# Kernel optimization log

Hardware: AMD Instinct MI355X
Metric: run time of the kernel (lower is better)

The kernel has to match this reference:

```python
import jax, jax.numpy as jnp
import numpy as np

N = 50000          # nodes
E = 800000         # edges
H = 64             # hidden_dim == node_embedding_dim (heads=1)
ED = 32            # edge_embedding_dim
L = 3              # num_layers - 1 TransformerConv layers
G = 256            # graphs in batch
NODE_CAT = 42
EDGE_CAT = 10
OUT = 32
SCALE = 1.0 / np.sqrt(H)


def segment_softmax(logits, seg, num_segments):
    mx = jax.ops.segment_max(logits, seg, num_segments=num_segments)
    e = jnp.exp(logits - mx[seg])
    denom = jax.ops.segment_sum(e, seg, num_segments=num_segments)
    return e / denom[seg]


def setup_inputs() -> dict:
    key = jax.random.key(0)
    ks = jax.random.split(key, 16)

    def init(k, shape, fan_in):
        return (jax.random.normal(k, shape, jnp.float32) / np.sqrt(fan_in))

    inp = {}
    inp["x"] = jax.random.randint(ks[0], (N,), 0, NODE_CAT)
    inp["edge_index"] = jax.random.randint(ks[1], (2, E), 0, N)
    inp["edge_attr"] = jax.random.randint(ks[2], (E,), 0, EDGE_CAT)
    inp["batch"] = jnp.sort(jax.random.randint(ks[3], (N,), 0, G))

    inp["node_emb"] = init(ks[4], (NODE_CAT, H), 1)
    inp["edge_emb"] = init(ks[5], (EDGE_CAT, ED), 1)
    # stacked per-layer TransformerConv params (input dim is H for all layers
    # since node_embedding_dim == hidden_dim)
    inp["Wq"] = init(ks[6], (L, H, H), H)
    inp["Wk"] = init(ks[7], (L, H, H), H)
    inp["Wv"] = init(ks[8], (L, H, H), H)
    inp["We"] = init(ks[9], (L, ED, H), ED)   # lin_edge, bias=False in PyG
    inp["Wskip"] = init(ks[10], (L, H, H), H)
    inp["bq"] = jnp.zeros((L, H), jnp.float32)
    inp["bk"] = jnp.zeros((L, H), jnp.float32)
    inp["bv"] = jnp.zeros((L, H), jnp.float32)
    inp["bskip"] = jnp.zeros((L, H), jnp.float32)
    # attentional aggregation readout
    inp["gate_W"] = init(ks[11], (H, 1), H)
    inp["gate_b"] = jnp.zeros((1,), jnp.float32)
    inp["out_W"] = init(ks[12], (H, OUT), H)
    inp["out_b"] = jnp.zeros((OUT,), jnp.float32)
    return inp


def reference(x, edge_index, edge_attr, batch, node_emb, edge_emb,
              Wq, Wk, Wv, We, Wskip, bq, bk, bv, bskip,
              gate_W, gate_b, out_W, out_b):
    src, dst = edge_index[0], edge_index[1]
    h = node_emb[x]            # [N, H] node embedding lookup
    e_feat = edge_emb[edge_attr]  # [E, ED] edge embedding lookup

    for l in range(L):
        q = h @ Wq[l] + bq[l]          # [N, H]
        k = h @ Wk[l] + bk[l]
        v = h @ Wv[l] + bv[l]
        e = e_feat @ We[l]             # [E, H]
        k_j = k[src] + e               # key_j += lin_edge(edge_attr)
        alpha = jnp.sum(q[dst] * k_j, axis=-1) * SCALE   # [E]
        a = segment_softmax(alpha, dst, N)               # softmax over dst nbhd
        msg = (v[src] + e) * a[:, None]                  # [E, H]
        agg = jax.ops.segment_sum(msg, dst, num_segments=N)
        h = jax.nn.relu(agg + h @ Wskip[l] + bskip[l])   # root/skip + ReLU

    # AttentionalAggregation: gate = gate_nn(x); x = nn(x); softmax gate per graph
    gate = (h @ gate_W + gate_b)[:, 0]   # [N]
    y = h @ out_W + out_b                # [N, OUT]
    g = segment_softmax(gate, batch, G)  # [N]
    return jax.ops.segment_sum(g[:, None] * y, batch, num_segments=G)  # [G, OUT]
```

## Files before the change

kernel.cpp:

```cpp
#include <hip/hip_runtime.h>
#include <hip/hip_bf16.h>

#define N_NODES 50000
#define N_EDGES 800000
#define H 64
#define ED 32
#define LAYERS 3
#define NGRAPH 256
#define OUTD 32
#define SCALE 0.125f
#define NCAT 42

#define BNODES 128
#define NBUCK 391
#define NB_HISTB 256
#define EPB (N_EDGES / NB_HISTB)

#define FB_HIST 256
#define FB_TE   8
#define FB_GB   2
#define FB_WB   192
#define FB_TAB  NCAT
#define NB_FRONT (FB_HIST + FB_TE + FB_GB + FB_WB + FB_TAB)

#define NB_SCAN   98
#define NB_AGG    3125
#define PKCAP     768

typedef __attribute__((ext_vector_type(8))) short bf16x8;
typedef __attribute__((ext_vector_type(4))) float f32x4;
typedef unsigned short ushort_t;

__device__ __forceinline__ unsigned f2bf(float f) {
    unsigned u = __float_as_uint(f);
    return (u + 0x7FFFu + ((u >> 16) & 1u)) >> 16;
}

__device__ __forceinline__ float radd16(float x) {
    x += __int_as_float(__builtin_amdgcn_update_dpp(0, __float_as_int(x), 0xB1, 0xF, 0xF, true));
    x += __int_as_float(__builtin_amdgcn_update_dpp(0, __float_as_int(x), 0x4E, 0xF, 0xF, true));
    x += __int_as_float(__builtin_amdgcn_update_dpp(0, __float_as_int(x), 0x124, 0xF, 0xF, true));
    x += __int_as_float(__builtin_amdgcn_update_dpp(0, __float_as_int(x), 0x128, 0xF, 0xF, true));
    return x;
}

__device__ __forceinline__ void build_bstart(const int* __restrict__ tot,
                                             int* bst, int* part, int t) {
    int u0 = t * 2, u1 = t * 2 + 1;
    int a0 = (u0 < NBUCK) ? tot[u0] : 0;
    int a1 = (u1 < NBUCK) ? tot[u1] : 0;
    part[t] = a0 + a1;
    __syncthreads();
    for (int off = 1; off < 256; off <<= 1) {
        int add = (t >= off) ? part[t - off] : 0;
        __syncthreads();
        part[t] += add;
        __syncthreads();
    }
    int excl = part[t] - (a0 + a1);
    if (u0 < NBUCK) bst[u0] = excl;
    if (u1 < NBUCK) bst[u1] = excl + a0;
    if (t == 0) bst[NBUCK] = N_EDGES;
    __syncthreads();
}

__global__ __launch_bounds__(256) void k_front(
    const int* __restrict__ x, const float* __restrict__ node_emb,
    const float* __restrict__ edge_emb, const float* __restrict__ We, float* __restrict__ te,
    const int* __restrict__ ei, int* __restrict__ hist,
    const int* __restrict__ batch, int* __restrict__ gs,
    const float* __restrict__ Wq, const float* __restrict__ Wk,
    const float* __restrict__ Wv, const float* __restrict__ Wsk,
    const float* __restrict__ bq, const float* __restrict__ bk,
    const float* __restrict__ bv, const float* __restrict__ bsk,
    ushort_t* __restrict__ wb16,
    unsigned* __restrict__ tqs, unsigned* __restrict__ tkv)
{
    __shared__ int lh[NBUCK];
    __shared__ float tb[4][64];
    int b = blockIdx.x, t = threadIdx.x;
    if (b < FB_HIST) {
        for (int i = t; i < NBUCK; i += 256) lh[i] = 0;
        __syncthreads();
        const int* dstp = ei + N_EDGES + b * EPB;
        for (int i = t; i < EPB; i += 256)
            atomicAdd(&lh[dstp[i] >> 7], 1);
        __syncthreads();
        for (int i = t; i < NBUCK; i += 256) hist[i * NB_HISTB + b] = lh[i];
    } else if (b < FB_HIST + FB_TE) {
        int i = (b - FB_HIST) * 256 + t;
        if (i < LAYERS * 10 * H) {
            int c = i & 63;
            int cat = (i >> 6) % 10;
            int l = i / (10 * H);
            float acc = 0.f;
            for (int d = 0; d < ED; d++)
                acc += edge_emb[cat * ED + d] * We[((size_t)l * ED + d) * H + c];
            te[i] = acc;
        }
    } else if (b < FB_HIST + FB_TE + FB_GB) {
        int g = (b - FB_HIST - FB_TE) * 256 + t;
        if (g <= NGRAPH) {
            int lo = 0, hi = N_NODES;
            while (lo < hi) {
                int mid = (lo + hi) >> 1;
                if (batch[mid] < g) lo = mid + 1; else hi = mid;
            }
            gs[g] = lo;
        }
    } else if (b < FB_HIST + FB_TE + FB_GB + FB_WB) {
        int g = (b - FB_HIST - FB_TE - FB_GB) * 256 + t;
        int l = g >> 14;
        int rem = g & 16383;
        int c_id = rem >> 11;
        int rr = (rem >> 3) & 255;
        int j = rem & 7;
        int mat = rr >> 6, n = rr & 63;
        int k = ((c_id >> 2) << 5) + ((c_id & 3) << 3) + j;
        const float* Wm = (mat == 0) ? Wq : (mat == 1) ? Wk : (mat == 2) ? Wv : Wsk;
        wb16[g] = (ushort_t)f2bf(Wm[(size_t)l * 4096 + k * 64 + n]);
    } else {
        int cat = b - (FB_HIST + FB_TE + FB_GB + FB_WB);
        int mat = t >> 6, c = t & 63;
        const float* Wm = (mat == 0) ? Wq : (mat == 1) ? Wk : (mat == 2) ? Wv : Wsk;
        const float* bm = (mat == 0) ? bq : (mat == 1) ? bk : (mat == 2) ? bv : bsk;
        float acc = bm[c];
        for (int k = 0; k < H; k++)
            acc += node_emb[cat * H + k] * Wm[k * 64 + c];
        tb[mat][c] = acc;
        __syncthreads();
        if (t < 64) {
            tqs[cat * 64 + t] = f2bf(tb[0][t]) | (f2bf(tb[3][t]) << 16);
            tkv[cat * 64 + t] = f2bf(tb[2][t]) | (f2bf(tb[1][t]) << 16);
        }
    }
}

__global__ __launch_bounds__(256) void k_scan(int* __restrict__ hist, int* __restrict__ tot)
{
    __shared__ int sv[256];
    int sb = blockIdx.x, t = threadIdx.x;
    for (int r = 0; r < 4; r++) {
        int u = sb * 4 + r;
        if (u < NBUCK) {
            int v = hist[u * NB_HISTB + t];
            sv[t] = v;
            __syncthreads();
            for (int off = 1; off < 256; off <<= 1) {
                int add = (t >= off) ? sv[t - off] : 0;
                __syncthreads();
                sv[t] += add;
                __syncthreads();
            }
            int incl = sv[t];
            hist[u * NB_HISTB + t] = incl - v;
            if (t == 255) tot[u] = incl;
            __syncthreads();
        }
    }
}

__global__ __launch_bounds__(256) void k_scatter(
    const int* __restrict__ ei, const int* __restrict__ ea, const int* __restrict__ x,
    const int* __restrict__ hist, const int* __restrict__ tot,
    int* __restrict__ pmid)
{
    __shared__ int bst[NBUCK + 1];
    __shared__ int part[256];
    __shared__ int curS[NBUCK];
    int b = blockIdx.x, t = threadIdx.x;
    build_bstart(tot, bst, part, t);
    for (int u = t; u < NBUCK; u += 256)
        curS[u] = bst[u] + hist[u * NB_HISTB + b];
    __syncthreads();
    int e0 = b * EPB;
    for (int i = t; i < EPB; i += 256) {
        int e = e0 + i;
        int src = ei[e], dst = ei[N_EDGES + e], cat = ea[e];
        int xs = x[src];
        int pos = atomicAdd(&curS[dst >> 7], 1);
        pmid[pos] = src | ((cat * NCAT + xs) << 16) | ((dst & 127) << 25);
    }
}

__global__ __launch_bounds__(256) void k_final(
    const int* __restrict__ pmid, const int* __restrict__ tot,
    int* __restrict__ packed, int* __restrict__ row_start, int* __restrict__ row_end)
{
    __shared__ int bst[NBUCK + 1];
    __shared__ int part[256];
    __shared__ int cnt[BNODES];
    __shared__ int scan_s[BNODES];
    int b = blockIdx.x, t = threadIdx.x;
    build_bstart(tot, bst, part, t);
    int beg = bst[b], end = bst[b + 1];
    if (t < BNODES) cnt[t] = 0;
    __syncthreads();
    for (int e = beg + t; e < end; e += 256)
        atomicAdd(&cnt[((unsigned)pmid[e] >> 25) & 127], 1);
    __syncthreads();
    if (t < BNODES) scan_s[t] = cnt[t];
    __syncthreads();
    for (int off = 1; off < BNODES; off <<= 1) {
        int add = (t >= off && t < BNODES) ? scan_s[t - off] : 0;
        __syncthreads();
        if (t < BNODES) scan_s[t] += add;
        __syncthreads();
    }
    if (t < BNODES) {
        int c = cnt[t];
        int excl = scan_s[t] - c;
        int node = b * BNODES + t;
        if (node < N_NODES) {
            row_start[node] = beg + excl;
            row_end[node] = beg + excl + c;
        }
        cnt[t] = beg + excl;
    }
    __syncthreads();
    for (int e = beg + t; e < end; e += 256) {
        int p = pmid[e];
        int pos = atomicAdd(&cnt[((unsigned)p >> 25) & 127], 1);
        packed[pos] = p & 0x1FFFFFF;
    }
}

struct EdgeLd { uint4 kv; float4 t; };
__device__ __forceinline__ float edge_dot(const EdgeLd& e, const float4& q4) {
    float p;
    p = (__uint_as_float(e.kv.x & 0xFFFF0000u) + e.t.x) * q4.x;
    p = fmaf(__uint_as_float(e.kv.y & 0xFFFF0000u) + e.t.y, q4.y, p);
    p = fmaf(__uint_as_float(e.kv.z & 0xFFFF0000u) + e.t.z, q4.z, p);
    p = fmaf(__uint_as_float(e.kv.w & 0xFFFF0000u) + e.t.w, q4.w, p);
    return radd16(p) * SCALE;
}
__device__ __forceinline__ float4 edge_val(const EdgeLd& e) {
    float4 v;
    v.x = __uint_as_float(e.kv.x << 16) + e.t.x;
    v.y = __uint_as_float(e.kv.y << 16) + e.t.y;
    v.z = __uint_as_float(e.kv.z << 16) + e.t.z;
    v.w = __uint_as_float(e.kv.w << 16) + e.t.w;
    return v;
}

template<int MODE>
__device__ __forceinline__ void agg_body(
    const int* __restrict__ row_start, const int* __restrict__ row_end,
    const int* __restrict__ packed, const int* __restrict__ x,
    const unsigned* __restrict__ qs_in, const unsigned* __restrict__ kv_in,
    const unsigned* __restrict__ tqs, const unsigned* __restrict__ tkv,
    const float* __restrict__ te,
    const ushort_t* __restrict__ wbn, const float* __restrict__ bqn,
    const float* __restrict__ bkn, const float* __restrict__ bvn,
    const float* __restrict__ bsn,
    unsigned* __restrict__ qs_out, unsigned* __restrict__ kv_out,
    float* __restrict__ hf, const float* __restrict__ gW,
    const float* __restrict__ gb, float* __restrict__ gate,
    float* tel, ushort_t* hs16, int* pkl)
{
    int t = threadIdx.x, bid = blockIdx.x;
    int wave = t >> 6, lane = t & 63;
    int g = lane >> 4, i16 = lane & 15;
    int dst = bid * 16 + wave * 4 + g;
    int beg = row_start[dst], end = row_end[dst];
    int beg0 = row_start[bid * 16];
    int cnt = row_end[bid * 16 + 15] - beg0;
    bool use_lds = (cnt <= PKCAP);
    for (int i = t; i < 640; i += 256) tel[i] = te[i];
    if (use_lds) for (int i = t; i < cnt; i += 256) pkl[i] = packed[beg0 + i];
    uint4 uq;
    if constexpr (MODE == 0)
        uq = *(const uint4*)(tqs + (x[dst] << 6) + (i16 << 2));
    else
        uq = *(const uint4*)(qs_in + (size_t)dst * 64 + (i16 << 2));
    __syncthreads();
    float4 q4, s4;
    q4.x = __uint_as_float(uq.x << 16); s4.x = __uint_as_float(uq.x & 0xFFFF0000u);
    q4.y = __uint_as_float(uq.y << 16); s4.y = __uint_as_float(uq.y & 0xFFFF0000u);
    q4.z = __uint_as_float(uq.z << 16); s4.z = __uint_as_float(uq.z & 0xFFFF0000u);
    q4.w = __uint_as_float(uq.w << 16); s4.w = __uint_as_float(uq.w & 0xFFFF0000u);
    float m = -1e30f, l = 0.f;
    float4 acc = {0.f, 0.f, 0.f, 0.f};

    auto eload = [&](int pkt) {
        EdgeLd r;
        unsigned catx = ((unsigned)pkt >> 16) & 0x1FFu;
        int cat = (int)((catx * 1561u) >> 16);
        r.t = *(const float4*)(tel + (cat << 6) + (i16 << 2));
        if constexpr (MODE == 0) {
            int xc = (int)catx - cat * NCAT;
            r.kv = *(const uint4*)(tkv + (xc << 6) + (i16 << 2));
        } else {
            int src = pkt & 0xFFFF;
            r.kv = *(const uint4*)(kv_in + ((size_t)src << 6) + (i16 << 2));
        }
        return r;
    };
    auto run = [&](auto PKT) {
        int e = beg;
        for (; e + 3 < end; e += 4) {
            int p0 = PKT(e), p1 = PKT(e + 1), p2 = PKT(e + 2), p3 = PKT(e + 3);
            EdgeLd e0 = eload(p0), e1 = eload(p1), e2 = eload(p2), e3 = eload(p3);
            float a0 = edge_dot(e0, q4), a1 = edge_dot(e1, q4);
            float a2 = edge_dot(e2, q4), a3 = edge_dot(e3, q4);
            float mn = fmaxf(m, fmaxf(fmaxf(a0, a1), fmaxf(a2, a3)));
            float corr = __expf(m - mn);
            float w0 = __expf(a0 - mn), w1 = __expf(a1 - mn);
            float w2 = __expf(a2 - mn), w3 = __expf(a3 - mn);
            float4 v0 = edge_val(e0), v1 = edge_val(e1), v2 = edge_val(e2), v3 = edge_val(e3);
            acc.x = fmaf(w0, v0.x, fmaf(w1, v1.x, fmaf(w2, v2.x, fmaf(w3, v3.x, acc.x * corr))));
            acc.y = fmaf(w0, v0.y, fmaf(w1, v1.y, fmaf(w2, v2.y, fmaf(w3, v3.y, acc.y * corr))));
            acc.z = fmaf(w0, v0.z, fmaf(w1, v1.z, fmaf(w2, v2.z, fmaf(w3, v3.z, acc.z * corr))));
            acc.w = fmaf(w0, v0.w, fmaf(w1, v1.w, fmaf(w2, v2.w, fmaf(w3, v3.w, acc.w * corr))));
            l = fmaf(l, corr, (w0 + w1) + (w2 + w3));
            m = mn;
        }
        for (; e < end; e++) {
            EdgeLd e0 = eload(PKT(e));
            float a = edge_dot(e0, q4);
            float mn = fmaxf(m, a);
            float corr = __expf(m - mn);
            float w = __expf(a - mn);
            float4 v4 = edge_val(e0);
            acc.x = fmaf(w, v4.x, acc.x * corr);
            acc.y = fmaf(w, v4.y, acc.y * corr);
            acc.z = fmaf(w, v4.z, acc.z * corr);
            acc.w = fmaf(w, v4.w, acc.w * corr);
            l = fmaf(l, corr, w);
            m = mn;
        }
    };
    if (use_lds) run([&](int e) { return pkl[e - beg0]; });
    else         run([&](int e) { return packed[e]; });

    float inv = (l > 0.f) ? 1.f / l : 0.f;
    float4 hv;
    hv.x = fmaxf(acc.x * inv + s4.x, 0.f);
    hv.y = fmaxf(acc.y * inv + s4.y, 0.f);
    hv.z = fmaxf(acc.z * inv + s4.z, 0.f);
    hv.w = fmaxf(acc.w * inv + s4.w, 0.f);
    if constexpr (MODE == 2) {
        *(float4*)(hf + (size_t)dst * H + (i16 << 2)) = hv;
        float4 g4 = *(const float4*)(gW + (i16 << 2));
        float p = hv.x * g4.x + hv.y * g4.y + hv.z * g4.z + hv.w * g4.w;
        p = radd16(p);
        if (i16 == 0) gate[dst] = p + gb[0];
    } else {
        uint2 hp;
        hp.x = f2bf(hv.x) | (f2bf(hv.y) << 16);
        hp.y = f2bf(hv.z) | (f2bf(hv.w) << 16);
        *(uint2*)(hs16 + (((wave * 4 + g) << 6) + (i16 << 2))) = hp;
        __syncthreads();
        int n16 = lane & 15, quad = lane >> 4;
        f32x4 oacc[4];
        #pragma unroll
        for (int i = 0; i < 4; i++) oacc[i] = (f32x4){0.f, 0.f, 0.f, 0.f};
        #pragma unroll
        for (int kb = 0; kb < 2; kb++) {
            bf16x8 afr = *(const bf16x8*)(hs16 + ((n16 << 6) + kb * 32 + quad * 8));
            #pragma unroll
            for (int mat = 0; mat < 4; mat++) {
                int ct = mat * 4 + wave;
                const bf16x8* bp = (const bf16x8*)(wbn + (((kb * 4 + quad) << 11) + ((ct * 16 + n16) << 3)));
                oacc[mat] = __builtin_amdgcn_mfma_f32_16x16x32_bf16(afr, *bp, oacc[mat], 0, 0, 0);
            }
        }
        int col = (wave << 4) + n16;
        float bQ = bqn[col], bK = bkn[col], bV = bvn[col], bS = bsn[col];
        int nb = bid * 16 + quad * 4;
        #pragma unroll
        for (int r = 0; r < 4; r++) {
            qs_out[(size_t)(nb + r) * 64 + col] = f2bf(oacc[0][r] + bQ) | (f2bf(oacc[3][r] + bS) << 16);
            kv_out[(size_t)(nb + r) * 64 + col] = f2bf(oacc[2][r] + bV) | (f2bf(oacc[1][r] + bK) << 16);
        }
    }
}

__global__ __launch_bounds__(256, 6) void k_agg0(
    const int* __restrict__ row_start, const int* __restrict__ row_end,
    const int* __restrict__ packed, const int* __restrict__ x,
    const unsigned* __restrict__ tqs, const unsigned* __restrict__ tkv,
    const float* __restrict__ te,
    const ushort_t* __restrict__ wbn, const float* __restrict__ bqn,
    const float* __restrict__ bkn, const float* __restrict__ bvn,
    const float* __restrict__ bsn,
    unsigned* __restrict__ qs_out, unsigned* __restrict__ kv_out)
{
    __shared__ float tel[640];
    __shared__ ushort_t hs16[1024];
    __shared__ int pkl[PKCAP];
    agg_body<0>(row_start, row_end, packed, x, nullptr, nullptr, tqs, tkv, te,
                wbn, bqn, bkn, bvn, bsn, qs_out, kv_out,
                nullptr, nullptr, nullptr, nullptr, tel, hs16, pkl);
}

__global__ __launch_bounds__(256, 6) void k_agg1(
    const int* __restrict__ row_start, const int* __restrict__ row_end,
    const int* __restrict__ packed,
    const unsigned* __restrict__ qs_in, const unsigned* __restrict__ kv_in,
    const float* __restrict__ te,
    const ushort_t* __restrict__ wbn, const float* __restrict__ bqn,
    const float* __restrict__ bkn, const float* __restrict__ bvn,
    const float* __restrict__ bsn,
    unsigned* __restrict__ qs_out, unsigned* __restrict__ kv_out)
{
    __shared__ float tel[640];
    __shared__ ushort_t hs16[1024];
    __shared__ int pkl[PKCAP];
    agg_body<1>(row_start, row_end, packed, nullptr, qs_in, kv_in, nullptr, nullptr, te,
                wbn, bqn, bkn, bvn, bsn, qs_out, kv_out,
                nullptr, nullptr, nullptr, nullptr, tel, hs16, pkl);
}

__global__ __launch_bounds__(256, 6) void k_agg2(
    const int* __restrict__ row_start, const int* __restrict__ row_end,
    const int* __restrict__ packed,
    const unsigned* __restrict__ qs_in, const unsigned* __restrict__ kv_in,
    const float* __restrict__ te,
    float* __restrict__ hf, const float* __restrict__ gW,
    const float* __restrict__ gb, float* __restrict__ gate)
{
    __shared__ float tel[640];
    __shared__ int pkl[PKCAP];
    agg_body<2>(row_start, row_end, packed, nullptr, qs_in, kv_in, nullptr, nullptr, te,
                nullptr, nullptr, nullptr, nullptr, nullptr, nullptr, nullptr,
                hf, gW, gb, gate, tel, nullptr, pkl);
}

__global__ __launch_bounds__(256) void k_readout2(
    const float* __restrict__ h, const float* __restrict__ oW,
    const float* __restrict__ ob, const float* __restrict__ gate,
    const int* __restrict__ gs, float* __restrict__ out)
{
    __shared__ float hs[8][H + 1];
    __shared__ float red[256];
    __shared__ float den_s[8];
    __shared__ float gmax_s, den_tot;
    int t = threadIdx.x;
    int g = blockIdx.x;
    int ln = t >> 5, o = t & 31;
    float wreg[H];
    #pragma unroll
    for (int i = 0; i < H; i++) wreg[i] = oW[i * OUTD + o];
    int beg = gs[g], end = gs[g + 1];
    float mx = -INFINITY;
    for (int n = beg + t; n < end; n += 256) mx = fmaxf(mx, gate[n]);
    red[t] = mx;
    __syncthreads();
    for (int sft = 128; sft > 0; sft >>= 1) {
        if (t < sft) red[t] = fmaxf(red[t], red[t + sft]);
        __syncthreads();
    }
    if (t == 0) gmax_s = red[0];
    __syncthreads();
    float gm = gmax_s;
    float acc = 0.f, den = 0.f;
    for (int n0 = beg; n0 < end; n0 += 8) {
        __syncthreads();
        for (int i = t; i < 8 * H; i += 256) {
            int r = i >> 6, c = i & 63;
            int n = n0 + r;
            hs[r][c] = (n < end) ? h[(size_t)n * H + c] : 0.f;
        }
        __syncthreads();
        int n = n0 + ln;
        if (n < end) {
            float wt = __expf(gate[n] - gm);
            float d0 = 0.f;
            #pragma unroll
            for (int i = 0; i < H; i++) d0 += hs[ln][i] * wreg[i];
            acc += wt * d0;
            if (o == 0) den += wt;
        }
    }
    __syncthreads();
    red[t] = acc;
    if (o == 0) den_s[ln] = den;
    __syncthreads();
    for (int sft = 4; sft >= 1; sft >>= 1) {
        if (ln < sft) red[t] += red[t + sft * 32];
        __syncthreads();
    }
    if (t == 0) {
        float dt = 0.f;
        #pragma unroll
        for (int i = 0; i < 8; i++) dt += den_s[i];
        den_tot = dt;
    }
    __syncthreads();
    if (ln == 0) {
        float dt = den_tot;
        out[g * OUTD + o] = (dt > 0.f) ? red[o] / dt + ob[o] : 0.f;
    }
}

extern "C" void kernel_launch(void* const* d_in, const int* in_sizes, int n_in,
                              void* d_out, int out_size, void* d_ws, size_t ws_size,
                              hipStream_t stream)
{
    const int* x        = (const int*)d_in[0];
    const int* ei       = (const int*)d_in[1];
    const int* ea       = (const int*)d_in[2];
    const int* batch    = (const int*)d_in[3];
    const float* node_emb = (const float*)d_in[4];
    const float* edge_emb = (const float*)d_in[5];
    const float* Wq    = (const float*)d_in[6];
    const float* Wk    = (const float*)d_in[7];
    const float* Wv    = (const float*)d_in[8];
    const float* We    = (const float*)d_in[9];
    const float* Wskip = (const float*)d_in[10];
    const float* bq    = (const float*)d_in[11];
    const float* bk    = (const float*)d_in[12];
    const float* bv    = (const float*)d_in[13];
    const float* bskip = (const float*)d_in[14];
    const float* gate_W = (const float*)d_in[15];
    const float* gate_b = (const float*)d_in[16];
    const float* out_W  = (const float*)d_in[17];
    const float* out_b  = (const float*)d_in[18];
    float* out = (float*)d_out;

    const size_t NH = (size_t)N_NODES * H;
    float* ws   = (float*)d_ws;
    unsigned* qs_a = (unsigned*)ws;
    unsigned* kv_a = qs_a + NH;
    unsigned* qs_b = kv_a + NH;
    unsigned* kv_b = qs_b + NH;
    float* hf32 = (float*)(kv_b + NH);
    float* te   = hf32 + NH;
    float* gate = te + LAYERS * 10 * H;
    int* row_start = (int*)(gate + N_NODES);
    int* row_end   = row_start + N_NODES;
    int* packed    = row_end + N_NODES;
    int* pmid      = packed + N_EDGES;
    int* hist      = pmid + N_EDGES;
    int* tot       = hist + NBUCK * NB_HISTB;
    int* gs        = tot + NBUCK;
    unsigned* tqs  = (unsigned*)(gs + NGRAPH + 1);
    unsigned* tkv  = tqs + FB_TAB * 64;
    ushort_t* wb16 = (ushort_t*)(tkv + FB_TAB * 64);

    k_front<<<NB_FRONT, 256, 0, stream>>>(x, node_emb, edge_emb, We, te, ei, hist, batch, gs,
                                          Wq, Wk, Wv, Wskip, bq, bk, bv, bskip, wb16, tqs, tkv);
    k_scan<<<NB_SCAN, 256, 0, stream>>>(hist, tot);
    k_scatter<<<NB_HISTB, 256, 0, stream>>>(ei, ea, x, hist, tot, pmid);
    k_final<<<NBUCK, 256, 0, stream>>>(pmid, tot, packed, row_start, row_end);

    k_agg0<<<NB_AGG, 256, 0, stream>>>(
        row_start, row_end, packed, x, tqs, tkv, te,
        wb16 + (size_t)1 * 16384, bq + H, bk + H, bv + H, bskip + H, qs_a, kv_a);
    k_agg1<<<NB_AGG, 256, 0, stream>>>(
        row_start, row_end, packed, qs_a, kv_a, te + 10 * H,
        wb16 + (size_t)2 * 16384, bq + 2 * H, bk + 2 * H, bv + 2 * H, bskip + 2 * H, qs_b, kv_b);
    k_agg2<<<NB_AGG, 256, 0, stream>>>(
        row_start, row_end, packed, qs_b, kv_b, te + 2 * 10 * H,
        hf32, gate_W, gate_b, gate);

    k_readout2<<<NGRAPH, 256, 0, stream>>>(hf32, out_W, out_b, gate, gs, out);
}
```

Measured before the change: 257.3 us.

## Fuse graph readout into last aggregation kernel via last-block-done counters

Removes the separate readout kernel launch by having each k_agg2 block decrement a per-graph counter of 16-node chunks after writing its outputs. The block that finishes a graph's last chunk then does the gated softmax readout for that graph. The per-graph counters are computed in the front kernel with binary searches over batch. This saves a launch and lets readout overlap with the tail of aggregation. In exchange it adds atomics, fences, and extra shared memory that may lower occupancy of the aggregation kernel, and readout work is serialized onto whichever blocks finish last.

```diff
diff --git a/kernel.cpp b/kernel.cpp
--- a/kernel.cpp
+++ b/kernel.cpp
@@ -64,11 +64,20 @@
     __syncthreads();
 }
 
+__device__ __forceinline__ int bsearch_batch(const int* __restrict__ batch, int g) {
+    int lo = 0, hi = N_NODES;
+    while (lo < hi) {
+        int mid = (lo + hi) >> 1;
+        if (batch[mid] < g) lo = mid + 1; else hi = mid;
+    }
+    return lo;
+}
+
 __global__ __launch_bounds__(256) void k_front(
     const int* __restrict__ x, const float* __restrict__ node_emb,
     const float* __restrict__ edge_emb, const float* __restrict__ We, float* __restrict__ te,
     const int* __restrict__ ei, int* __restrict__ hist,
-    const int* __restrict__ batch, int* __restrict__ gs,
+    const int* __restrict__ batch, int* __restrict__ gs, int* __restrict__ gcnt,
     const float* __restrict__ Wq, const float* __restrict__ Wk,
     const float* __restrict__ Wv, const float* __restrict__ Wsk,
     const float* __restrict__ bq, const float* __restrict__ bk,
@@ -101,12 +110,12 @@
     } else if (b < FB_HIST + FB_TE + FB_GB) {
         int g = (b - FB_HIST - FB_TE) * 256 + t;
         if (g <= NGRAPH) {
-            int lo = 0, hi = N_NODES;
-            while (lo < hi) {
-                int mid = (lo + hi) >> 1;
-                if (batch[mid] < g) lo = mid + 1; else hi = mid;
-            }
+            int lo = bsearch_batch(batch, g);
             gs[g] = lo;
+            if (g < NGRAPH) {
+                int hi2 = bsearch_batch(batch, g + 1);
+                gcnt[g] = ((hi2 - 1) >> 4) - (lo >> 4) + 1;
+            }
         }
     } else if (b < FB_HIST + FB_TE + FB_GB + FB_WB) {
         int g = (b - FB_HIST - FB_TE - FB_GB) * 256 + t;
@@ -418,79 +427,93 @@
     const unsigned* __restrict__ qs_in, const unsigned* __restrict__ kv_in,
     const float* __restrict__ te,
     float* __restrict__ hf, const float* __restrict__ gW,
-    const float* __restrict__ gb, float* __restrict__ gate)
+    const float* __restrict__ gb, float* __restrict__ gate,
+    const int* __restrict__ batch, int* __restrict__ gcnt,
+    const int* __restrict__ gs, const float* __restrict__ oW,
+    const float* __restrict__ ob, float* __restrict__ out)
 {
     __shared__ float tel[640];
     __shared__ int pkl[PKCAP];
+    __shared__ float wls[H * OUTD];
+    __shared__ float hsr[8][H + 1];
+    __shared__ float red[256];
+    __shared__ float den_s[8];
+    __shared__ float gmax_s, den_tot;
+    __shared__ int sinfo[2];
+
     agg_body<2>(row_start, row_end, packed, nullptr, qs_in, kv_in, nullptr, nullptr, te,
                 nullptr, nullptr, nullptr, nullptr, nullptr, nullptr, nullptr,
                 hf, gW, gb, gate, tel, nullptr, pkl);
-}
-
-__global__ __launch_bounds__(256) void k_readout2(
-    const float* __restrict__ h, const float* __restrict__ oW,
-    const float* __restrict__ ob, const float* __restrict__ gate,
-    const int* __restrict__ gs, float* __restrict__ out)
-{
-    __shared__ float hs[8][H + 1];
-    __shared__ float red[256];
-    __shared__ float den_s[8];
-    __shared__ float gmax_s, den_tot;
+
     int t = threadIdx.x;
-    int g = blockIdx.x;
-    int ln = t >> 5, o = t & 31;
-    float wreg[H];
-    #pragma unroll
-    for (int i = 0; i < H; i++) wreg[i] = oW[i * OUTD + o];
-    int beg = gs[g], end = gs[g + 1];
-    float mx = -INFINITY;
-    for (int n = beg + t; n < end; n += 256) mx = fmaxf(mx, gate[n]);
-    red[t] = mx;
-    __syncthreads();
-    for (int sft = 128; sft > 0; sft >>= 1) {
-        if (t < sft) red[t] = fmaxf(red[t], red[t + sft]);
-        __syncthreads();
-    }
-    if (t == 0) gmax_s = red[0];
-    __syncthreads();
-    float gm = gmax_s;
-    float acc = 0.f, den = 0.f;
-    for (int n0 = beg; n0 < end; n0 += 8) {
-        __syncthreads();
-        for (int i = t; i < 8 * H; i += 256) {
-            int r = i >> 6, c = i & 63;
-            int n = n0 + r;
-            hs[r][c] = (n < end) ? h[(size_t)n * H + c] : 0.f;
-        }
-        __syncthreads();
-        int n = n0 + ln;
-        if (n < end) {
-            float wt = __expf(gate[n] - gm);
-            float d0 = 0.f;
-            #pragma unroll
-            for (int i = 0; i < H; i++) d0 += hs[ln][i] * wreg[i];
-            acc += wt * d0;
-            if (o == 0) den += wt;
-        }
-    }
-    __syncthreads();
-    red[t] = acc;
-    if (o == 0) den_s[ln] = den;
-    __syncthreads();
-    for (int sft = 4; sft >= 1; sft >>= 1) {
-        if (ln < sft) red[t] += red[t + sft * 32];
-        __syncthreads();
-    }
-    if (t == 0) {
-        float dt = 0.f;
-        #pragma unroll
-        for (int i = 0; i < 8; i++) dt += den_s[i];
-        den_tot = dt;
-    }
-    __syncthreads();
-    if (ln == 0) {
-        float dt = den_tot;
-        out[g * OUTD + o] = (dt > 0.f) ? red[o] / dt + ob[o] : 0.f;
+    __syncthreads();
+    if (t == 0) { sinfo[0] = batch[blockIdx.x * 16]; sinfo[1] = batch[blockIdx.x * 16 + 15]; }
+    __syncthreads();
+    int ga = sinfo[0], gb2 = sinfo[1];
+    __builtin_amdgcn_fence(__ATOMIC_RELEASE, "agent");
+    for (int g = ga; g <= gb2; ++g) {
+        if (t == 0)
+            sinfo[0] = __hip_atomic_fetch_add(&gcnt[g], -1, __ATOMIC_ACQ_REL,
+                                              __HIP_MEMORY_SCOPE_AGENT);
+        __syncthreads();
+        bool last = (sinfo[0] == 1);
+        __syncthreads();
+        if (last) {
+            __builtin_amdgcn_fence(__ATOMIC_ACQUIRE, "agent");
+            int ln = t >> 5, o = t & 31;
+            for (int i = t; i < H * OUTD; i += 256) wls[i] = oW[i];
+            int beg = gs[g], end = gs[g + 1];
+            float mx = -INFINITY;
+            for (int n = beg + t; n < end; n += 256) mx = fmaxf(mx, gate[n]);
+            red[t] = mx;
+            __syncthreads();
+            for (int sft = 128; sft > 0; sft >>= 1) {
+                if (t < sft) red[t] = fmaxf(red[t], red[t + sft]);
+                __syncthreads();
+            }
+            if (t == 0) gmax_s = red[0];
+            __syncthreads();
+            float gm = gmax_s;
+            float acc = 0.f, den = 0.f;
+            for (int n0 = beg; n0 < end; n0 += 8) {
+                __syncthreads();
+                for (int i = t; i < 8 * H; i += 256) {
+                    int r = i >> 6, c = i & 63;
+                    int n = n0 + r;
+                    hsr[r][c] = (n < end) ? hf[(size_t)n * H + c] : 0.f;
+                }
+                __syncthreads();
+                int n = n0 + ln;
+                if (n < end) {
+                    float wt = __expf(gate[n] - gm);
+                    float d0 = 0.f;
+                    #pragma unroll
+                    for (int i = 0; i < H; i++) d0 += hsr[ln][i] * wls[i * OUTD + o];
+                    acc += wt * d0;
+                    if (o == 0) den += wt;
+                }
+            }
+            __syncthreads();
+            red[t] = acc;
+            if (o == 0) den_s[ln] = den;
+            __syncthreads();
+            for (int sft = 4; sft >= 1; sft >>= 1) {
+                if (ln < sft) red[t] += red[t + sft * 32];
+                __syncthreads();
+            }
+            if (t == 0) {
+                float dt = 0.f;
+                #pragma unroll
+                for (int i = 0; i < 8; i++) dt += den_s[i];
+                den_tot = dt;
+            }
+            __syncthreads();
+            if (ln == 0) {
+                float dt = den_tot;
+                out[g * OUTD + o] = (dt > 0.f) ? red[o] / dt + ob[o] : 0.f;
+            }
+        }
+        __syncthreads();
     }
 }
 
@@ -538,9 +561,11 @@
     unsigned* tqs  = (unsigned*)(gs + NGRAPH + 1);
     unsigned* tkv  = tqs + FB_TAB * 64;
     ushort_t* wb16 = (ushort_t*)(tkv + FB_TAB * 64);
-
-    k_front<<<NB_FRONT, 256, 0, stream>>>(x, node_emb, edge_emb, We, te, ei, hist, batch, gs,
-                                          Wq, Wk, Wv, Wskip, bq, bk, bv, bskip, wb16, tqs, tkv);
+    int* gcnt      = (int*)(wb16 + 3 * 16384);
+
+    k_front<<<NB_FRONT, 256, 0, stream>>>(x, node_emb, edge_emb, We, te, ei, hist, batch,
+                                          gs, gcnt, Wq, Wk, Wv, Wskip, bq, bk, bv, bskip,
+                                          wb16, tqs, tkv);
     k_scan<<<NB_SCAN, 256, 0, stream>>>(hist, tot);
     k_scatter<<<NB_HISTB, 256, 0, stream>>>(ei, ea, x, hist, tot, pmid);
     k_final<<<NBUCK, 256, 0, stream>>>(pmid, tot, packed, row_start, row_end);
@@ -553,7 +578,5 @@
         wb16 + (size_t)2 * 16384, bq + 2 * H, bk + 2 * H, bv + 2 * H, bskip + 2 * H, qs_b, kv_b);
     k_agg2<<<NB_AGG, 256, 0, stream>>>(
         row_start, row_end, packed, qs_b, kv_b, te + 2 * 10 * H,
-        hf32, gate_W, gate_b, gate);
-
-    k_readout2<<<NGRAPH, 256, 0, stream>>>(hf32, out_W, out_b, gate, gs, out);
-}
+        hf32, gate_W, gate_b, gate, batch, gcnt, gs, out_W, out_b, out);
+}
```

Measured after the change: 674.0 us. 2.62x slower.
